# Kernel tuning notes

Hardware: AMD Instinct MI355X
Metric: run time of the kernel (lower is better)

The kernel has to match this reference:

```python
import jax, jax.numpy as jnp
import numpy as np

NUM_DOF = 7
NUM_STEPS = 100
T = 0.02
V_MAX, A_MAX, J_MAX, P_MAX = 1.0, 2.0, 5.0, 3.14
MAXITER = 20
RHO = 1.0
BATCH = 1024
HIDDEN = 1024
NVAR = NUM_DOF * NUM_STEPS            # 700
NUM_ACC = NUM_STEPS - 1
NUM_JERK = NUM_ACC - 1
NUM_POS = NUM_STEPS
NVC = 2 * NUM_STEPS * NUM_DOF         # vel constraints
NAC = 2 * NUM_ACC * NUM_DOF
NJC = 2 * NUM_JERK * NUM_DOF
NPC = 2 * NUM_POS * NUM_DOF
M_CON = NVC + NAC + NJC + NPC         # 5558 total constraints
OUT_DIM = 2 * NVAR + M_CON            # 6958 mlp output dim

def _build_mats():
    P_vel = np.eye(NUM_STEPS)
    P_acc = np.diff(P_vel, axis=0) / T
    P_jerk = np.diff(P_acc, axis=0) / T
    P_pos = np.cumsum(P_vel, axis=0) * T
    ud = lambda P: np.vstack((P, -P))
    I = np.eye(NUM_DOF)
    A_control = np.vstack([np.kron(I, ud(P)) for P in (P_vel, P_acc, P_jerk, P_pos)])
    bnd = np.zeros((1, NUM_STEPS)); bnd[0, 0] = 1.0
    A_eq = np.kron(I, bnd)
    cost = np.eye(NVAR) + RHO * (A_control.T @ A_control)  # A_projection = I
    Q = np.block([[cost, A_eq.T], [A_eq, np.zeros((NUM_DOF, NUM_DOF))]])
    Q_inv = np.linalg.inv(Q)
    return jnp.asarray(A_control, jnp.float32), jnp.asarray(Q_inv, jnp.float32)

A_CONTROL, Q_INV = _build_mats()


def setup_inputs() -> dict:
    key = jax.random.key(0)
    k1, k2, k3, k4, k5 = jax.random.split(key, 5)
    return {
        "input_nn": jax.random.normal(k1, (BATCH, NVAR), jnp.float32),
        "theta_init": jax.random.uniform(k2, (BATCH, 1), jnp.float32),
        "v_start": jax.random.normal(k3, (BATCH, NUM_DOF), jnp.float32),
        "W1": jax.random.normal(k4, (NVAR, HIDDEN), jnp.float32) / np.sqrt(NVAR).astype(np.float32),
        "b1": jnp.zeros((HIDDEN,), jnp.float32),
        "W2": jax.random.normal(k5, (HIDDEN, OUT_DIM), jnp.float32) / np.sqrt(HIDDEN).astype(np.float32),
        "b2": jnp.zeros((OUT_DIM,), jnp.float32),
    }


def reference(input_nn, theta_init, v_start, W1, b1, W2, b2):
    # robust normalization (torch.median on even batch = lower middle element)
    med = jnp.quantile(input_nn, 0.5, axis=0, method="lower")
    q1 = jnp.quantile(input_nn, 0.25, axis=0)
    q3 = jnp.quantile(input_nn, 0.75, axis=0)
    iqr = q3 - q1
    iqr = jnp.where(iqr == 0, jnp.asarray(1.0, iqr.dtype), iqr)
    inp_norm = (input_nn - med) / iqr

    # mlp decoder
    h = jax.nn.relu(inp_norm @ W1 + b1)
    out = h @ W2 + b2
    xi0 = out[:, :NVAR]
    lam0 = out[:, NVAR:2 * NVAR]
    s0 = jnp.maximum(0.0, out[:, 2 * NVAR:2 * NVAR + M_CON])

    xi_samples = input_nn[:, :NVAR]
    B = input_nn.shape[0]
    dt = input_nn.dtype
    b_control = jnp.concatenate([
        V_MAX * jnp.ones((B, NVC), dt),
        A_MAX * jnp.ones((B, NAC), dt),
        J_MAX * jnp.ones((B, NJC), dt),
        (-theta_init + P_MAX) * jnp.ones((B, NPC // 2), dt),
        (theta_init + P_MAX) * jnp.ones((B, NPC // 2), dt),
    ], axis=1)  # [B, M_CON]
    b_eq = v_start  # [B, num_dof]

    def step(carry, _):
        xi, lam, s = carry
        b_aug = b_control - s
        # lincost = -lamda - xi_samples - rho * A_control^T b_aug   (A_projection = I)
        lincost = -lam - xi_samples - RHO * (b_aug @ A_CONTROL)
        rhs = jnp.concatenate([-lincost, b_eq], axis=1)        # [B, nvar+dof]
        sol = rhs @ Q_INV.T
        xi_new = sol[:, :NVAR]
        Ax = xi_new @ A_CONTROL.T                              # [B, M_CON]
        s_new = jnp.maximum(0.0, b_control - Ax)
        res_vec = Ax - b_control + s_new
        res_norm = jnp.linalg.norm(res_vec, axis=1)
        lam_new = lam - RHO * (res_vec @ A_CONTROL)
        fp = jnp.linalg.norm(lam - lam_new, axis=1) + jnp.linalg.norm(s - s_new, axis=1)
        return (xi_new, lam_new, s_new), (res_norm, fp)

    (xi_f, _, _), (primal_res, fixed_res) = jax.lax.scan(step, (xi0, lam0, s0), None, length=MAXITER)
    avg_primal = jnp.sum(primal_res, axis=0) / MAXITER
    avg_fixed = jnp.sum(fixed_res, axis=0) / MAXITER
    return xi_f, avg_fixed, avg_primal, primal_res, fixed_res
```

## Files before the change

kernel.cpp:

```cpp
#include <hip/hip_runtime.h>

#define NVARS 700
#define MC    5558
#define MAXIT 20

typedef __attribute__((ext_vector_type(8))) short bf16x8;
typedef __attribute__((ext_vector_type(4))) float f32x4;

__device__ __forceinline__ ushort f2bf(float x) {
  unsigned u = __float_as_uint(x);
  return (ushort)((u + 0x7FFFu + ((u >> 16) & 1u)) >> 16);
}

__device__ __forceinline__ double Wfun(int a, int b) {
  if (a < 0 || a > 99 || b < 0 || b > 99) return 0.0;
  int d = a - b; if (d < 0) d = -d;
  int l = a < b ? a : b;
  const double iT2 = 2500.0;
  const double iT4 = 6250000.0;
  double w = 0.0;
  if (d == 0) {
    w = 3.0;
    w += 2.0 * iT2 * (double)((a <= 98 ? 1 : 0) + (a >= 1 ? 1 : 0));
    double dd = (double)(((a - 2) >= 0 && (a - 2) <= 97) ? 1 : 0)
              + 4.0 * (double)(((a - 1) >= 0 && (a - 1) <= 97) ? 1 : 0)
              + (double)((a <= 97) ? 1 : 0);
    w += 2.0 * iT4 * dd;
  } else if (d == 1) {
    w = -2.0 * iT2;
    double dd = -2.0 * (double)(((l - 1) >= 0 && (l - 1) <= 97) ? 1 : 0)
                - 2.0 * (double)((l <= 97) ? 1 : 0);
    w += 2.0 * iT4 * dd;
  } else if (d == 2) {
    w = 2.0 * iT4 * (double)((l <= 97) ? 1 : 0);
  }
  return w;
}

__global__ __launch_bounds__(128) void qinv_kernel(double* __restrict__ zbuf,
                                                   double* __restrict__ cid,
                                                   float* __restrict__ Qt)
{
  __shared__ double Bb[100][4];
  __shared__ double Gb[100][4];
  __shared__ double invd[100];
  int tid = threadIdx.x;
  for (int q = tid; q < 400; q += 128) {
    int i = q >> 2, k = q & 3;
    int j = i - k;
    double v = 0.0;
    if (j >= 0) {
      v = Wfun(i, j) - Wfun(i + 1, j) - Wfun(i, j + 1) + Wfun(i + 1, j + 1);
      if (k == 0) v += 2.0 * 0.02 * 0.02;
    }
    Bb[i][k] = v;
  }
  __syncthreads();
  if (tid == 0) {
    for (int i = 0; i < 100; ++i) {
      for (int k = 3; k >= 1; --k) {
        int j = i - k;
        if (j < 0) { Gb[i][k] = 0.0; continue; }
        double s = Bb[i][k];
        for (int m = k + 1; m <= 3; ++m)
          if (m <= i) s -= Gb[i][m] * Gb[j][m - k];
        Gb[i][k] = s * invd[j];
      }
      double s = Bb[i][0];
      for (int m = 1; m <= 3; ++m)
        if (m <= i) s -= Gb[i][m] * Gb[i][m];
      double g = sqrt(s);
      Gb[i][0] = g;
      invd[i] = 1.0 / g;
    }
  }
  __syncthreads();
  if (tid < 100) {
    int c = tid;
    double z0 = 0, z1 = 0, z2 = 0;
    for (int i = 0; i < 100; ++i) {
      double v = (i == c ? 1.0 : 0.0) - (i == (c - 1) ? 1.0 : 0.0);
      double s = v - Gb[i][1] * z0 - Gb[i][2] * z1 - Gb[i][3] * z2;
      double z = s * invd[i];
      zbuf[i * 128 + c] = z;
      z2 = z1; z1 = z0; z0 = z;
    }
    double y0 = 0, y1 = 0, y2 = 0;
    for (int i = 99; i >= 0; --i) {
      double s = zbuf[i * 128 + c];
      if (i + 1 <= 99) s -= Gb[i + 1][1] * y0;
      if (i + 2 <= 99) s -= Gb[i + 2][2] * y1;
      if (i + 3 <= 99) s -= Gb[i + 3][3] * y2;
      double y = s * invd[i];
      zbuf[i * 128 + c] = y;
      y2 = y1; y1 = y0; y0 = y;
    }
    double ym = 0.0;
    for (int i = 0; i < 100; ++i) {
      double y = zbuf[i * 128 + c];
      cid[i * 100 + c] = y - ym;
      ym = y;
    }
  }
  __syncthreads();
  double invs = 1.0 / cid[0];
  for (int q = tid; q < 101 * 100; q += 128) {
    int k = q / 100, i = q - (q / 100) * 100;
    double val;
    if (k < 100) val = cid[i * 100 + k] - cid[i * 100] * cid[k] * invs;
    else         val = cid[i * 100] * invs;
    Qt[k * 100 + i] = (float)val;
  }
}

__global__ __launch_bounds__(256) void quantile_kernel(const float* __restrict__ in,
                                                       float* __restrict__ med,
                                                       float* __restrict__ rinv)
{
  __shared__ float v[1024];
  int c = blockIdx.x, tid = threadIdx.x;
  for (int i = tid; i < 1024; i += 256) v[i] = in[i * NVARS + c];
  __syncthreads();
  for (int k = 2; k <= 1024; k <<= 1) {
    for (int j = k >> 1; j > 0; j >>= 1) {
      for (int i = tid; i < 1024; i += 256) {
        int ixj = i ^ j;
        if (ixj > i) {
          float a = v[i], b2 = v[ixj];
          bool up = ((i & k) == 0);
          if ((a > b2) == up) { v[i] = b2; v[ixj] = a; }
        }
      }
      __syncthreads();
    }
  }
  if (tid == 0) {
    float m  = v[511];
    float q1 = v[255] + 0.75f * (v[256] - v[255]);
    float q3 = v[767] + 0.25f * (v[768] - v[767]);
    float iq = q3 - q1;
    if (iq == 0.f) iq = 1.f;
    med[c] = m;
    rinv[c] = 1.f / iq;
  }
}

__global__ __launch_bounds__(256) void normalize_split(const float* __restrict__ in,
                                                       const float* __restrict__ med,
                                                       const float* __restrict__ rinv,
                                                       ushort* __restrict__ Ah,
                                                       ushort* __restrict__ Al)
{
  int idx = blockIdx.x * 256 + threadIdx.x;
  if (idx >= 1024 * 704) return;
  int r = idx / 704, c = idx - r * 704;
  float v = 0.f;
  if (c < 700) v = (in[r * NVARS + c] - med[c]) * rinv[c];
  ushort h = f2bf(v);
  float fh = __uint_as_float(((unsigned)h) << 16);
  Ah[idx] = h;
  Al[idx] = f2bf(v - fh);
}

__global__ __launch_bounds__(256) void tsplit(const float* __restrict__ src,
                                              int srows, int scols, int sld, int col0,
                                              ushort* __restrict__ dh,
                                              ushort* __restrict__ dl, int dld)
{
  __shared__ float tile[32][33];
  int k0 = blockIdx.x * 32, n0 = blockIdx.y * 32;
  int tx = threadIdx.x, ty = threadIdx.y;
  for (int i = ty; i < 32; i += 8) {
    int k = k0 + i, c = col0 + n0 + tx;
    tile[i][tx] = (k < srows && c < scols) ? src[(size_t)k * sld + c] : 0.f;
  }
  __syncthreads();
  for (int i = ty; i < 32; i += 8) {
    int n = n0 + i, k = k0 + tx;
    float v = tile[tx][i];
    ushort h = f2bf(v);
    float fh = __uint_as_float(((unsigned)h) << 16);
    dh[(size_t)n * dld + k] = h;
    dl[(size_t)n * dld + k] = f2bf(v - fh);
  }
}

template <int BM, int BN, int MODE>
__global__ __launch_bounds__(256) void gemm_mfma(
    const ushort* __restrict__ Agh, const ushort* __restrict__ Agl,
    const ushort* __restrict__ Bgh, const ushort* __restrict__ Bgl,
    const float* __restrict__ bias, int bias_n,
    float* __restrict__ Cf, ushort* __restrict__ Chi, ushort* __restrict__ Clo,
    int Kp, int ldc)
{
  constexpr int ACH = BM * 4 / 256;
  constexpr int BCH = BN * 4 / 256;
  constexpr int MF = BM / 32;
  constexpr int NF = BN / 32;
  __shared__ __align__(16) ushort Ash[BM * 40];
  __shared__ __align__(16) ushort Asl[BM * 40];
  __shared__ __align__(16) ushort Bsh[BN * 40];
  __shared__ __align__(16) ushort Bsl[BN * 40];

  const int t = threadIdx.x;
  const size_t bm = (size_t)blockIdx.y * BM;
  const size_t bn = (size_t)blockIdx.x * BN;

  size_t aoff[ACH]; int awo[ACH];
#pragma unroll
  for (int s = 0; s < ACH; ++s) {
    int slot = t * ACH + s, row = slot >> 2, ch = slot & 3;
    aoff[s] = (bm + row) * (size_t)Kp + ch * 8;
    awo[s] = row * 40 + ch * 8;
  }
  size_t boff[BCH]; int bwo[BCH];
#pragma unroll
  for (int s = 0; s < BCH; ++s) {
    int slot = t * BCH + s, row = slot >> 2, ch = slot & 3;
    boff[s] = (bn + row) * (size_t)Kp + ch * 8;
    bwo[s] = row * 40 + ch * 8;
  }

  const int w = t >> 6, lane = t & 63;
  const int wr = w >> 1, wc = w & 1;
  const int fr = lane & 15, fg = lane >> 4;

  f32x4 acc[MF][NF];
#pragma unroll
  for (int a = 0; a < MF; ++a)
#pragma unroll
    for (int b = 0; b < NF; ++b) acc[a][b] = (f32x4){0.f, 0.f, 0.f, 0.f};

  const int nk = Kp >> 5;
  uint4 rAh[ACH], rAl[ACH], rBh[BCH], rBl[BCH];
#pragma unroll
  for (int s = 0; s < ACH; ++s) { rAh[s] = *(const uint4*)(Agh + aoff[s]); rAl[s] = *(const uint4*)(Agl + aoff[s]); }
#pragma unroll
  for (int s = 0; s < BCH; ++s) { rBh[s] = *(const uint4*)(Bgh + boff[s]); rBl[s] = *(const uint4*)(Bgl + boff[s]); }

  for (int kt = 0;; ++kt) {
    __syncthreads();
#pragma unroll
    for (int s = 0; s < ACH; ++s) { *(uint4*)&Ash[awo[s]] = rAh[s]; *(uint4*)&Asl[awo[s]] = rAl[s]; }
#pragma unroll
    for (int s = 0; s < BCH; ++s) { *(uint4*)&Bsh[bwo[s]] = rBh[s]; *(uint4*)&Bsl[bwo[s]] = rBl[s]; }
    __syncthreads();
    if (kt + 1 < nk) {
      int ko = (kt + 1) * 32;
#pragma unroll
      for (int s = 0; s < ACH; ++s) { rAh[s] = *(const uint4*)(Agh + aoff[s] + ko); rAl[s] = *(const uint4*)(Agl + aoff[s] + ko); }
#pragma unroll
      for (int s = 0; s < BCH; ++s) { rBh[s] = *(const uint4*)(Bgh + boff[s] + ko); rBl[s] = *(const uint4*)(Bgl + boff[s] + ko); }
    }
    bf16x8 fah[MF], fal[MF], fbh[NF], fbl[NF];
#pragma unroll
    for (int mf = 0; mf < MF; ++mf) {
      int off = (wr * (BM / 2) + mf * 16 + fr) * 40 + fg * 8;
      fah[mf] = *(const bf16x8*)&Ash[off];
      fal[mf] = *(const bf16x8*)&Asl[off];
    }
#pragma unroll
    for (int nf = 0; nf < NF; ++nf) {
      int off = (wc * (BN / 2) + nf * 16 + fr) * 40 + fg * 8;
      fbh[nf] = *(const bf16x8*)&Bsh[off];
      fbl[nf] = *(const bf16x8*)&Bsl[off];
    }
#pragma unroll
    for (int mf = 0; mf < MF; ++mf)
#pragma unroll
      for (int nf = 0; nf < NF; ++nf) {
        acc[mf][nf] = __builtin_amdgcn_mfma_f32_16x16x32_bf16(fah[mf], fbh[nf], acc[mf][nf], 0, 0, 0);
        acc[mf][nf] = __builtin_amdgcn_mfma_f32_16x16x32_bf16(fah[mf], fbl[nf], acc[mf][nf], 0, 0, 0);
        acc[mf][nf] = __builtin_amdgcn_mfma_f32_16x16x32_bf16(fal[mf], fbh[nf], acc[mf][nf], 0, 0, 0);
      }
    if (kt + 1 >= nk) break;
  }

#pragma unroll
  for (int mf = 0; mf < MF; ++mf)
#pragma unroll
    for (int nf = 0; nf < NF; ++nf) {
      int col = (int)bn + wc * (BN / 2) + nf * 16 + fr;
      int rowb = (int)bm + wr * (BM / 2) + mf * 16 + fg * 4;
#pragma unroll
      for (int j = 0; j < 4; ++j) {
        int row = rowb + j;
        float v = acc[mf][nf][j];
        if (MODE == 0) {
          float bv = (col < bias_n) ? bias[col] : 0.f;
          Cf[(size_t)row * ldc + col] = v + bv;
        } else {
          float r = fmaxf(v + bias[col], 0.f);
          ushort h = f2bf(r);
          float fh = __uint_as_float(((unsigned)h) << 16);
          Chi[(size_t)row * ldc + col] = h;
          Clo[(size_t)row * ldc + col] = f2bf(r - fh);
        }
      }
    }
}

__global__ __launch_bounds__(256) void normalize_kernel(const float* __restrict__ in,
                                                        const float* __restrict__ med,
                                                        const float* __restrict__ rinv,
                                                        float* __restrict__ An)
{
  int idx = blockIdx.x * 256 + threadIdx.x;
  if (idx < 1024 * NVARS) {
    int c = idx % NVARS;
    An[idx] = (in[idx] - med[c]) * rinv[c];
  }
}

template <bool RELU>
__global__ __launch_bounds__(256) void gemm_kernel(const float* __restrict__ A, int lda,
                                                   const float* __restrict__ B, int ldb,
                                                   const float* __restrict__ bias,
                                                   float* __restrict__ C, int ldc,
                                                   int N, int K)
{
  __shared__ __align__(16) float As[16][68];
  __shared__ __align__(16) float Bs[16][64];
  int tid = threadIdx.x;
  int bm = blockIdx.y * 64, bn = blockIdx.x * 64;
  int tx = tid & 15, ty = tid >> 4;
  float acc[4][4] = {};
  for (int k0 = 0; k0 < K; k0 += 16) {
    {
      int q = tid * 4;
      int m = q >> 4, kk = q & 15;
      const float* ap = A + (size_t)(bm + m) * lda + k0;
#pragma unroll
      for (int s2 = 0; s2 < 4; ++s2) {
        int kc = kk + s2;
        As[kc][m] = (k0 + kc < K) ? ap[kc] : 0.f;
      }
    }
#pragma unroll
    for (int s2 = 0; s2 < 4; ++s2) {
      int q = tid + s2 * 256;
      int kk = q >> 6, n = q & 63;
      float val = 0.f;
      if (k0 + kk < K && bn + n < N) val = B[(size_t)(k0 + kk) * ldb + bn + n];
      Bs[kk][n] = val;
    }
    __syncthreads();
#pragma unroll
    for (int kk = 0; kk < 16; ++kk) {
      float4 av = *reinterpret_cast<const float4*>(&As[kk][ty * 4]);
      float4 bv = *reinterpret_cast<const float4*>(&Bs[kk][tx * 4]);
      acc[0][0] += av.x * bv.x; acc[0][1] += av.x * bv.y; acc[0][2] += av.x * bv.z; acc[0][3] += av.x * bv.w;
      acc[1][0] += av.y * bv.x; acc[1][1] += av.y * bv.y; acc[1][2] += av.y * bv.z; acc[1][3] += av.y * bv.w;
      acc[2][0] += av.z * bv.x; acc[2][1] += av.z * bv.y; acc[2][2] += av.z * bv.z; acc[2][3] += av.z * bv.w;
      acc[3][0] += av.w * bv.x; acc[3][1] += av.w * bv.y; acc[3][2] += av.w * bv.z; acc[3][3] += av.w * bv.w;
    }
    __syncthreads();
  }
#pragma unroll
  for (int i = 0; i < 4; ++i) {
    int m = bm + ty * 4 + i;
#pragma unroll
    for (int j = 0; j < 4; ++j) {
      int n = bn + tx * 4 + j;
      if (n < N) {
        float r = acc[i][j] + bias[n];
        if (RELU) r = fmaxf(r, 0.f);
        C[(size_t)m * ldc + n] = r;
      }
    }
  }
}

__device__ __forceinline__ float iscan(float v, int lane) {
#pragma unroll
  for (int off = 1; off < 64; off <<= 1) {
    float u = __shfl_up(v, off);
    v += (lane >= off) ? u : 0.f;
  }
  return v;
}

struct TR {
  float vp0, vm0, vp1, vm1;
  float ap0, am0, ap1, am1;
  float jp0, jm0, jp1, jm1;
  float pp0, pm0, pp1, pm1;
};

__device__ __forceinline__ void wpair(float tp, float tm, float& ws, float& wr) {
  float a = fmaxf(tp, 0.f), b = fmaxf(tm, 0.f);
  ws = b - a;
  wr = (tm - tp) - ws;
}

__device__ __forceinline__ void w_phase(const TR& t, int l, bool hi, float dth,
                                        float& os0, float& os1, float& or0, float& or1)
{
  float vs0, vr0, vs1, vr1, ys0, yr0, ys1, yr1;
  float zs0, zr0, zs1, zr1, ps0, pr0, ps1, pr1;
  wpair(t.vp0, t.vm0, vs0, vr0);
  wpair(t.ap0, t.am0, ys0, yr0);
  wpair(t.jp0, t.jm0, zs0, zr0);
  wpair(t.pp0, t.pm0, ps0, pr0);
  if (hi) { wpair(t.vp1, t.vm1, vs1, vr1); wpair(t.pp1, t.pm1, ps1, pr1); }
  else    { vs1 = vr1 = ps1 = pr1 = 0.f; }
  if (hi && l <= 34) { wpair(t.ap1, t.am1, ys1, yr1); } else { ys1 = yr1 = 0.f; }
  if (hi && l <= 33) { wpair(t.jp1, t.jm1, zs1, zr1); } else { zs1 = zr1 = 0.f; }

  const int lm1 = (l + 63) & 63, lm2 = (l + 62) & 63;
  float u1ys0 = __shfl(ys0, lm1), u1ys1 = __shfl(ys1, lm1);
  float u1zs0 = __shfl(zs0, lm1), u1zs1 = __shfl(zs1, lm1);
  float u2zs0 = __shfl(zs0, lm2), u2zs1 = __shfl(zs1, lm2);
  float u1yr0 = __shfl(yr0, lm1), u1yr1 = __shfl(yr1, lm1);
  float u1zr0 = __shfl(zr0, lm1), u1zr1 = __shfl(zr1, lm1);
  float u2zr0 = __shfl(zr0, lm2), u2zr1 = __shfl(zr1, lm2);

  float pa0s = ps0 + dth;
  float pa1s = hi ? ps1 + dth : 0.f;
  float pa0r = pr0;
  float pa1r = hi ? pr1 : 0.f;
  float s0s = iscan(pa0s, l);
  float s0r = iscan(pa0r, l);
  float tots = __shfl(s0s, 63), totr = __shfl(s0r, 63);
  float s1s = iscan(pa1s, l) + tots;
  float s1r = iscan(pa1r, l) + totr;
  float Ss = __shfl(s1s, 35), Sr = __shfl(s1r, 35);
  float rc0s = Ss - s0s + pa0s, rc1s = Ss - s1s + pa1s;
  float rc0r = Sr - s0r + pa0r, rc1r = Sr - s1r + pa1r;

  float ym1s0 = l ? u1ys0 : 0.f, zm1s0 = l ? u1zs0 : 0.f, zm2s0 = (l >= 2) ? u2zs0 : 0.f;
  float ym1r0 = l ? u1yr0 : 0.f, zm1r0 = l ? u1zr0 : 0.f, zm2r0 = (l >= 2) ? u2zr0 : 0.f;
  os0 = vs0 + 50.f * (ym1s0 - ys0) + 2500.f * (zm2s0 - 2.f * zm1s0 + zs0) + 0.02f * rc0s;
  or0 = vr0 + 50.f * (ym1r0 - yr0) + 2500.f * (zm2r0 - 2.f * zm1r0 + zr0) + 0.02f * rc0r;
  float ym1s1 = l ? u1ys1 : u1ys0, zm1s1 = l ? u1zs1 : u1zs0, zm2s1 = (l >= 2) ? u2zs1 : u2zs0;
  float ym1r1 = l ? u1yr1 : u1yr0, zm1r1 = l ? u1zr1 : u1zr0, zm2r1 = (l >= 2) ? u2zr1 : u2zr0;
  os1 = vs1 + 50.f * (ym1s1 - ys1) + 2500.f * (zm2s1 - 2.f * zm1s1 + zs1) + 0.02f * rc1s;
  or1 = vr1 + 50.f * (ym1r1 - yr1) + 2500.f * (zm2r1 - 2.f * zm1r1 + zr1) + 0.02f * rc1r;
}

__global__ __launch_bounds__(448, 4) void solver_kernel(const float* __restrict__ out2,
                                                        const float* __restrict__ input,
                                                        const float* __restrict__ theta,
                                                        const float* __restrict__ vstart,
                                                        const float* __restrict__ Qtg,
                                                        float* __restrict__ out, int ldo)
{
  __shared__ __align__(16) float ru_t[101][12];
  __shared__ float pm[4][700];
  __shared__ float part[7][20][3];
  __shared__ float prfp[40];

  const int b = blockIdx.x, tid = threadIdx.x;
  const int d = tid >> 6, l = tid & 63;
  const bool hi = (l < 36);
  const int i2 = 64 + l;
  const float th = theta[b];
  const float dth = (d == 3) ? -2.f * th : 0.f;
  const float bp  = (d <= 3) ? (3.14f - th) : (3.14f + th);
  const float bm2 = (d <  3) ? (3.14f - th) : (3.14f + th);
  const float* orow = out2 + (size_t)b * ldo;
  const float* srow = orow + 700;

  float lam0 = orow[d * 100 + l];
  float xs0  = input[(size_t)b * NVARS + d * 100 + l];
  float lam1 = hi ? orow[d * 100 + i2] : 0.f;
  float xs1  = hi ? input[(size_t)b * NVARS + d * 100 + i2] : 0.f;

  TR t;
  {
    const int vb = d * 200, ab = 1400 + d * 198, jb = 2786 + d * 196, pb = 4158 + d * 200;
    t.vp0 = fmaxf(srow[vb + l], 0.f);        t.vm0 = fmaxf(srow[vb + 100 + l], 0.f);
    t.ap0 = fmaxf(srow[ab + l], 0.f);        t.am0 = fmaxf(srow[ab + 99 + l], 0.f);
    t.jp0 = fmaxf(srow[jb + l], 0.f);        t.jm0 = fmaxf(srow[jb + 98 + l], 0.f);
    t.pp0 = fmaxf(srow[pb + l], 0.f);        t.pm0 = fmaxf(srow[pb + 100 + l], 0.f);
    t.vp1 = hi        ? fmaxf(srow[vb + i2], 0.f)      : 0.f;
    t.vm1 = hi        ? fmaxf(srow[vb + 100 + i2], 0.f) : 0.f;
    t.ap1 = (l <= 34) ? fmaxf(srow[ab + i2], 0.f)      : 0.f;
    t.am1 = (l <= 34) ? fmaxf(srow[ab + 99 + i2], 0.f) : 0.f;
    t.jp1 = (l <= 33) ? fmaxf(srow[jb + i2], 0.f)      : 0.f;
    t.jm1 = (l <= 33) ? fmaxf(srow[jb + 98 + i2], 0.f) : 0.f;
    t.pp1 = hi        ? fmaxf(srow[pb + i2], 0.f)      : 0.f;
    t.pm1 = hi        ? fmaxf(srow[pb + 100 + i2], 0.f) : 0.f;
  }
  if (l == 0) ru_t[100][d] = vstart[b * 7 + d];

  {
    float os0, os1, or0, or1;
    w_phase(t, l, hi, dth, os0, os1, or0, or1);
    ru_t[l][d] = lam0 + xs0 + os0;
    if (hi) ru_t[i2][d] = lam1 + xs1 + os1;
  }

  for (int it = 0; it < MAXIT; ++it) {
    __syncthreads();
    {
      int kc = tid / 112, r = tid - kc * 112;
      if (r < 100) {
        float acc[7] = {0.f, 0.f, 0.f, 0.f, 0.f, 0.f, 0.f};
        int k0 = kc * 25, k1 = (kc == 3) ? 101 : k0 + 25;
        for (int k = k0; k < k1; ++k) {
          float qv = Qtg[k * 100 + r];
          float4 ra = *reinterpret_cast<const float4*>(&ru_t[k][0]);
          float4 rb = *reinterpret_cast<const float4*>(&ru_t[k][4]);
          acc[0] += qv * ra.x; acc[1] += qv * ra.y; acc[2] += qv * ra.z; acc[3] += qv * ra.w;
          acc[4] += qv * rb.x; acc[5] += qv * rb.y; acc[6] += qv * rb.z;
        }
#pragma unroll
        for (int dd = 0; dd < 7; ++dd) pm[kc][dd * 100 + r] = acc[dd];
      }
    }
    __syncthreads();
    {
      int p = tid;
      if (p < 700) { float v = pm[0][p] + pm[1][p] + pm[2][p] + pm[3][p]; pm[0][p] = v; }
      p = tid + 448;
      if (p < 700) { float v = pm[0][p] + pm[1][p] + pm[2][p] + pm[3][p]; pm[0][p] = v; }
    }
    __syncthreads();

    float r2 = 0.f, ds2 = 0.f, dl2 = 0.f;
    {
      const float* xid = &pm[0][d * 100];
      float x0 = xid[l];
      float x1 = hi ? xid[i2] : 0.f;
      const int lp1 = (l + 1) & 63, lp2 = (l + 2) & 63;
      float d1x0 = __shfl(x0, lp1), d1x1 = __shfl(x1, lp1);
      float d2x0 = __shfl(x0, lp2), d2x1 = __shfl(x1, lp2);
      float xp1_0 = (l == 63) ? d1x1 : d1x0;
      float xp2_0 = (l >= 62) ? d2x1 : d2x0;
      float xp1_1 = d1x1, xp2_1 = d2x1;
      float c0 = iscan(x0, l);
      float tt = __shfl(c0, 63);
      float c1 = iscan(hi ? x1 : 0.f, l) + tt;
#define NU(tp_, tm_, np_, nm_) { \
      float sop = fmaxf(tp_, 0.f), som = fmaxf(tm_, 0.f); \
      float snp = fmaxf(np_, 0.f), snm = fmaxf(nm_, 0.f); \
      float e1 = sop - snp, e2 = som - snm; ds2 += e1 * e1 + e2 * e2; \
      float q1 = snp - (np_), q2 = snm - (nm_); r2 += q1 * q1 + q2 * q2; \
      tp_ = np_; tm_ = nm_; }
      { float np = 1.f - x0, nm = 1.f + x0; NU(t.vp0, t.vm0, np, nm) }
      { float a = 50.f * (xp1_0 - x0); float np = 2.f - a, nm = 2.f + a; NU(t.ap0, t.am0, np, nm) }
      { float j = 2500.f * (xp2_0 - 2.f * xp1_0 + x0); float np = 5.f - j, nm = 5.f + j; NU(t.jp0, t.jm0, np, nm) }
      { float np = bp - 0.02f * c0, nm = bm2 + 0.02f * c0; NU(t.pp0, t.pm0, np, nm) }
      if (hi) {
        { float np = 1.f - x1, nm = 1.f + x1; NU(t.vp1, t.vm1, np, nm) }
        { float np = bp - 0.02f * c1, nm = bm2 + 0.02f * c1; NU(t.pp1, t.pm1, np, nm) }
      }
      if (l <= 34) { float a = 50.f * (xp1_1 - x1); float np = 2.f - a, nm = 2.f + a; NU(t.ap1, t.am1, np, nm) }
      if (l <= 33) { float j = 2500.f * (xp2_1 - 2.f * xp1_1 + x1); float np = 5.f - j, nm = 5.f + j; NU(t.jp1, t.jm1, np, nm) }
#undef NU
    }

    {
      float os0, os1, or0, or1;
      w_phase(t, l, hi, dth, os0, os1, or0, or1);
      lam0 -= or0; dl2 += or0 * or0;
      ru_t[l][d] = lam0 + xs0 + os0;
      if (hi) {
        lam1 -= or1; dl2 += or1 * or1;
        ru_t[i2][d] = lam1 + xs1 + os1;
      }
    }

#pragma unroll
    for (int o = 32; o > 0; o >>= 1) {
      r2  += __shfl_down(r2, o);
      ds2 += __shfl_down(ds2, o);
      dl2 += __shfl_down(dl2, o);
    }
    if (l == 0) { part[d][it][0] = r2; part[d][it][1] = ds2; part[d][it][2] = dl2; }
  }

  __syncthreads();
  {
    float* xout = out + (size_t)b * NVARS + d * 100;
    const float* xid = &pm[0][d * 100];
    xout[l] = xid[l];
    if (hi) xout[i2] = xid[i2];
  }
  if (tid < 20) {
    int it = tid;
    float R2 = 0.f, DS2 = 0.f, DL2 = 0.f;
    for (int dd = 0; dd < 7; ++dd) {
      R2 += part[dd][it][0]; DS2 += part[dd][it][1]; DL2 += part[dd][it][2];
    }
    float pr = sqrtf(R2), fp = sqrtf(DL2) + sqrtf(DS2);
    out[718848 + it * 1024 + b] = pr;
    out[739328 + it * 1024 + b] = fp;
    prfp[it] = pr; prfp[20 + it] = fp;
  }
  __syncthreads();
  if (tid == 0) {
    float ap = 0.f, af = 0.f;
    for (int it = 0; it < 20; ++it) { ap += prfp[it]; af += prfp[20 + it]; }
    out[716800 + b] = af / 20.f;
    out[717824 + b] = ap / 20.f;
  }
}

extern "C" void kernel_launch(void* const* d_in, const int* in_sizes, int n_in,
                              void* d_out, int out_size, void* d_ws, size_t ws_size,
                              hipStream_t stream) {
  (void)in_sizes; (void)n_in; (void)out_size;
  const float* input  = (const float*)d_in[0];
  const float* theta  = (const float*)d_in[1];
  const float* vstart = (const float*)d_in[2];
  const float* W1     = (const float*)d_in[3];
  const float* b1     = (const float*)d_in[4];
  const float* W2     = (const float*)d_in[5];
  const float* b2     = (const float*)d_in[6];
  float* out = (float*)d_out;

  double* wsd  = (double*)d_ws;
  double* zbuf = wsd;
  double* cid  = wsd + 12800;
  float* wsf  = (float*)d_ws;
  float* Qt   = wsf + 45600;
  float* med  = wsf + 55704;
  float* rinv = wsf + 56408;

  hipLaunchKernelGGL(qinv_kernel, dim3(1), dim3(128), 0, stream, zbuf, cid, Qt);
  hipLaunchKernelGGL(quantile_kernel, dim3(700), dim3(256), 0, stream, input, med, rinv);

  const size_t HHI = 57112, HLO = 581400, W2TH = 1105688, W2TL = 4316952,
               OUT2 = 7528216, NEED = 13950744;
  const size_t ANH = OUT2, ANL = OUT2 + 360448, W1TH = OUT2 + 720896, W1TL = OUT2 + 1081344;

  if (ws_size >= NEED * 4ull) {
    ushort* an_h  = (ushort*)(wsf + ANH);
    ushort* an_l  = (ushort*)(wsf + ANL);
    ushort* w1t_h = (ushort*)(wsf + W1TH);
    ushort* w1t_l = (ushort*)(wsf + W1TL);
    ushort* h_h   = (ushort*)(wsf + HHI);
    ushort* h_l   = (ushort*)(wsf + HLO);
    ushort* w2t_h = (ushort*)(wsf + W2TH);
    ushort* w2t_l = (ushort*)(wsf + W2TL);
    float*  out2  = wsf + OUT2;

    hipLaunchKernelGGL(normalize_split, dim3((1024 * 704 + 255) / 256), dim3(256), 0, stream,
                       input, med, rinv, an_h, an_l);
    hipLaunchKernelGGL(tsplit, dim3(22, 32), dim3(32, 8), 0, stream,
                       W1, 700, 1024, 1024, 0, w1t_h, w1t_l, 704);
    hipLaunchKernelGGL(tsplit, dim3(32, 196), dim3(32, 8), 0, stream,
                       W2, 1024, 6958, 6958, 700, w2t_h, w2t_l, 1024);
    hipLaunchKernelGGL((gemm_mfma<64, 64, 1>), dim3(16, 16), dim3(256), 0, stream,
                       an_h, an_l, w1t_h, w1t_l, b1, 1024,
                       (float*)nullptr, h_h, h_l, 704, 1024);
    hipLaunchKernelGGL((gemm_mfma<128, 64, 0>), dim3(98, 8), dim3(256), 0, stream,
                       h_h, h_l, w2t_h, w2t_l, b2 + 700, 6258,
                       out2, (ushort*)nullptr, (ushort*)nullptr, 1024, 6272);
    hipLaunchKernelGGL(solver_kernel, dim3(1024), dim3(448), 0, stream,
                       out2, input, theta, vstart, Qt, out, 6272);
  } else {
    float* An   = wsf + 57112;
    float* h    = wsf + 773912;
    float* out2 = wsf + 1822488;
    if (ws_size < (size_t)(1822488 + 6408192) * 4) return;
    hipLaunchKernelGGL(normalize_kernel, dim3(2800), dim3(256), 0, stream, input, med, rinv, An);
    hipLaunchKernelGGL((gemm_kernel<true>), dim3(16, 16), dim3(256), 0, stream,
                       An, NVARS, W1, 1024, b1, h, 1024, 1024, NVARS);
    hipLaunchKernelGGL((gemm_kernel<false>), dim3(98, 16), dim3(256), 0, stream,
                       h, 1024, W2 + 700, 6958, b2 + 700, out2, 6258, 6258, 1024);
    hipLaunchKernelGGL(solver_kernel, dim3(1024), dim3(448), 0, stream,
                       out2, input, theta, vstart, Qt, out, 6258);
  }
}
```

Baseline: 660.0 us.

## Use DPP scans, fold partial-sum reduction, and enlarge MFMA GEMM tiles

Swaps the shuffle-based wave prefix scan for a DPP row-shift/row-broadcast scan and uses readlane for the broadcasts. It also drops the separate partial-sum pass and its barrier by summing the four pm slices where they are read, and replaces the shfl_down reductions with the scan's last lane. The MFMA GEMM tiles grow to 128x128 with half as many blocks. Risks: the DPP row_bcast encodings must be correct for CDNA wave64, the larger tiles leave few blocks to fill the CUs, and the four-slice sum is repeated at final output.

```diff
diff --git a/kernel.cpp b/kernel.cpp
--- a/kernel.cpp
+++ b/kernel.cpp
@@ -371,13 +371,26 @@
   }
 }
 
-__device__ __forceinline__ float iscan(float v, int lane) {
-#pragma unroll
-  for (int off = 1; off < 64; off <<= 1) {
-    float u = __shfl_up(v, off);
-    v += (lane >= off) ? u : 0.f;
-  }
-  return v;
+__device__ __forceinline__ float rdlane(float v, int lane) {
+  return __int_as_float(__builtin_amdgcn_readlane(__float_as_int(v), lane));
+}
+
+__device__ __forceinline__ float iscan(float v) {
+  float f = v;
+  int t;
+  t = __builtin_amdgcn_update_dpp(0, __float_as_int(f), 0x111, 0xf, 0xf, false);
+  f += __int_as_float(t);
+  t = __builtin_amdgcn_update_dpp(0, __float_as_int(f), 0x112, 0xf, 0xf, false);
+  f += __int_as_float(t);
+  t = __builtin_amdgcn_update_dpp(0, __float_as_int(f), 0x114, 0xf, 0xf, false);
+  f += __int_as_float(t);
+  t = __builtin_amdgcn_update_dpp(0, __float_as_int(f), 0x118, 0xf, 0xf, false);
+  f += __int_as_float(t);
+  t = __builtin_amdgcn_update_dpp(0, __float_as_int(f), 0x142, 0xa, 0xf, false);
+  f += __int_as_float(t);
+  t = __builtin_amdgcn_update_dpp(0, __float_as_int(f), 0x143, 0xc, 0xf, false);
+  f += __int_as_float(t);
+  return f;
 }
 
 struct TR {
@@ -419,12 +432,12 @@
   float pa1s = hi ? ps1 + dth : 0.f;
   float pa0r = pr0;
   float pa1r = hi ? pr1 : 0.f;
-  float s0s = iscan(pa0s, l);
-  float s0r = iscan(pa0r, l);
-  float tots = __shfl(s0s, 63), totr = __shfl(s0r, 63);
-  float s1s = iscan(pa1s, l) + tots;
-  float s1r = iscan(pa1r, l) + totr;
-  float Ss = __shfl(s1s, 35), Sr = __shfl(s1r, 35);
+  float s0s = iscan(pa0s);
+  float s0r = iscan(pa0r);
+  float tots = rdlane(s0s, 63), totr = rdlane(s0r, 63);
+  float s1s = iscan(pa1s) + tots;
+  float s1r = iscan(pa1r) + totr;
+  float Ss = rdlane(s1s, 35), Sr = rdlane(s1r, 35);
   float rc0s = Ss - s0s + pa0s, rc1s = Ss - s1s + pa1s;
   float rc0r = Sr - s0r + pa0r, rc1r = Sr - s1r + pa1r;
 
@@ -510,28 +523,25 @@
       }
     }
     __syncthreads();
-    {
-      int p = tid;
-      if (p < 700) { float v = pm[0][p] + pm[1][p] + pm[2][p] + pm[3][p]; pm[0][p] = v; }
-      p = tid + 448;
-      if (p < 700) { float v = pm[0][p] + pm[1][p] + pm[2][p] + pm[3][p]; pm[0][p] = v; }
-    }
-    __syncthreads();
 
     float r2 = 0.f, ds2 = 0.f, dl2 = 0.f;
     {
-      const float* xid = &pm[0][d * 100];
-      float x0 = xid[l];
-      float x1 = hi ? xid[i2] : 0.f;
+      const int a0 = d * 100 + l;
+      float x0 = pm[0][a0] + pm[1][a0] + pm[2][a0] + pm[3][a0];
+      float x1 = 0.f;
+      if (hi) {
+        const int a1 = d * 100 + i2;
+        x1 = pm[0][a1] + pm[1][a1] + pm[2][a1] + pm[3][a1];
+      }
       const int lp1 = (l + 1) & 63, lp2 = (l + 2) & 63;
       float d1x0 = __shfl(x0, lp1), d1x1 = __shfl(x1, lp1);
       float d2x0 = __shfl(x0, lp2), d2x1 = __shfl(x1, lp2);
       float xp1_0 = (l == 63) ? d1x1 : d1x0;
       float xp2_0 = (l >= 62) ? d2x1 : d2x0;
       float xp1_1 = d1x1, xp2_1 = d2x1;
-      float c0 = iscan(x0, l);
-      float tt = __shfl(c0, 63);
-      float c1 = iscan(hi ? x1 : 0.f, l) + tt;
+      float c0 = iscan(x0);
+      float tt = rdlane(c0, 63);
+      float c1 = iscan(hi ? x1 : 0.f) + tt;
 #define NU(tp_, tm_, np_, nm_) { \
       float sop = fmaxf(tp_, 0.f), som = fmaxf(tm_, 0.f); \
       float snp = fmaxf(np_, 0.f), snm = fmaxf(nm_, 0.f); \
@@ -562,21 +572,20 @@
       }
     }
 
-#pragma unroll
-    for (int o = 32; o > 0; o >>= 1) {
-      r2  += __shfl_down(r2, o);
-      ds2 += __shfl_down(ds2, o);
-      dl2 += __shfl_down(dl2, o);
-    }
-    if (l == 0) { part[d][it][0] = r2; part[d][it][1] = ds2; part[d][it][2] = dl2; }
+    r2 = iscan(r2); ds2 = iscan(ds2); dl2 = iscan(dl2);
+    if (l == 63) { part[d][it][0] = r2; part[d][it][1] = ds2; part[d][it][2] = dl2; }
   }
 
   __syncthreads();
   {
+    const int a0 = d * 100 + l;
+    float x0 = pm[0][a0] + pm[1][a0] + pm[2][a0] + pm[3][a0];
     float* xout = out + (size_t)b * NVARS + d * 100;
-    const float* xid = &pm[0][d * 100];
-    xout[l] = xid[l];
-    if (hi) xout[i2] = xid[i2];
+    xout[l] = x0;
+    if (hi) {
+      const int a1 = d * 100 + i2;
+      xout[i2] = pm[0][a1] + pm[1][a1] + pm[2][a1] + pm[3][a1];
+    }
   }
   if (tid < 20) {
     int it = tid;
@@ -643,10 +652,10 @@
                        W1, 700, 1024, 1024, 0, w1t_h, w1t_l, 704);
     hipLaunchKernelGGL(tsplit, dim3(32, 196), dim3(32, 8), 0, stream,
                        W2, 1024, 6958, 6958, 700, w2t_h, w2t_l, 1024);
-    hipLaunchKernelGGL((gemm_mfma<64, 64, 1>), dim3(16, 16), dim3(256), 0, stream,
+    hipLaunchKernelGGL((gemm_mfma<128, 128, 1>), dim3(8, 8), dim3(256), 0, stream,
                        an_h, an_l, w1t_h, w1t_l, b1, 1024,
                        (float*)nullptr, h_h, h_l, 704, 1024);
-    hipLaunchKernelGGL((gemm_mfma<128, 64, 0>), dim3(98, 8), dim3(256), 0, stream,
+    hipLaunchKernelGGL((gemm_mfma<128, 128, 0>), dim3(49, 8), dim3(256), 0, stream,
                        h_h, h_l, w2t_h, w2t_l, b2 + 700, 6258,
                        out2, (ushort*)nullptr, (ushort*)nullptr, 1024, 6272);
     hipLaunchKernelGGL(solver_kernel, dim3(1024), dim3(448), 0, stream,
```

Result: slower. 692.1 us (+4.9%).
